# Optimization experiments

Measured on AMD Instinct MI355X. Metric: run time of the kernel, lower is better.

The kernel has to match this reference:

```python
import jax, jax.numpy as jnp
import numpy as np

C1 = 384  # input channel dim (hardcoded in source)


def setup_inputs() -> dict:
    key = jax.random.key(0)
    kx, kq, kk, kv = jax.random.split(key, 4)
    B, T, C, H = 512, 256, C1, 64
    x = jax.random.normal(kx, (B, T, C), dtype=jnp.float32)
    # nn.Linear(C1, head_size, bias=False) weights, stored as (C, H) for x @ W
    Wq = jax.random.normal(kq, (C, H), dtype=jnp.float32) * (1.0 / np.sqrt(C))
    Wk = jax.random.normal(kk, (C, H), dtype=jnp.float32) * (1.0 / np.sqrt(C))
    Wv = jax.random.normal(kv, (C, H), dtype=jnp.float32) * (1.0 / np.sqrt(C))
    return {"x": x, "Wq": Wq, "Wk": Wk, "Wv": Wv}


def reference(x, Wq, Wk, Wv):
    B, T, C = x.shape
    q = jnp.einsum('btc,ch->bth', x, Wq)  # [B,T,H]
    k = jnp.einsum('btc,ch->bth', x, Wk)
    v = jnp.einsum('btc,ch->bth', x, Wv)
    # NOTE: source MULTIPLIES by C**0.5 (not the usual 1/sqrt(d)) -- faithful.
    scale = jnp.asarray(C, x.dtype) ** 0.5
    wei = jnp.einsum('bth,bsh->bts', q, k) * scale  # [B,T,T]
    causal = jnp.tril(jnp.ones((T, T), dtype=bool))
    wei = jnp.where(causal, wei, -jnp.inf)
    wei = jax.nn.softmax(wei, axis=-1)
    # dropout is identity in eval mode (deterministic reference)
    out = jnp.einsum('bts,bsh->bth', wei, v)  # [B,T,H]
    return out
```

## Files before the change

### kernel.cpp

```cpp
#include <hip/hip_runtime.h>
#include <hip/hip_bf16.h>
#include <math.h>

typedef _Float16 f16x8 __attribute__((ext_vector_type(8)));
typedef _Float16 f16x4 __attribute__((ext_vector_type(4)));
typedef _Float16 f16x2 __attribute__((ext_vector_type(2)));
typedef __fp16 fp16x2 __attribute__((ext_vector_type(2)));
typedef float f32x4 __attribute__((ext_vector_type(4)));

#define MFMA16(a, b, c) __builtin_amdgcn_mfma_f32_16x16x32_f16((a), (b), (c), 0, 0, 0)

typedef __attribute__((address_space(3))) char as3_char;
typedef __attribute__((address_space(1))) const char as1_char;
__device__ __forceinline__ void glds16(const void* g, void* l) {
  __builtin_amdgcn_global_load_lds((as1_char*)g, (as3_char*)l, 16, 0, 0);
}

union F16x8u { f16x8 v; f16x2 h[4]; };

__device__ __forceinline__ f16x2 pkrtz(float a, float b) {
  fp16x2 r = __builtin_amdgcn_cvt_pkrtz(a, b);
  return __builtin_bit_cast(f16x2, r);
}

__global__ __launch_bounds__(256) void wprep_kernel(
    const float* __restrict__ Wq, const float* __restrict__ Wk, const float* __restrict__ Wv,
    _Float16* __restrict__ wstg) {
  int s = blockIdx.x * 256 + threadIdx.x;
  int c0 = s / 1536, s2 = s % 1536;
  int p = s2 / 768, r = (s2 % 768) / 4, gg = s2 & 3;
  int g = gg ^ ((r >> 1) & 3);
  int sel = r >> 6, h = r & 63;
  const float* W = (sel == 0) ? Wq : (sel == 1) ? Wk : Wv;
  f16x8 o;
#pragma unroll
  for (int e = 0; e < 8; ++e) {
    float val = W[(c0 * 32 + g * 8 + e) * 64 + h];
    _Float16 hi = (_Float16)val;
    o[e] = p ? (_Float16)(val - (float)hi) : hi;
  }
  *(f16x8*)&wstg[(size_t)s * 8] = o;
}

__global__ __launch_bounds__(1024) void fused_kernel(
    const float* __restrict__ x,
    const _Float16* __restrict__ wstg,
    float* __restrict__ out) {
  __shared__ __align__(16) char smem[156672];
  _Float16* kh = (_Float16*)smem;
  _Float16* kl = (_Float16*)(smem + 36864);
  _Float16* vT = (_Float16*)(smem + 73728);
  char* wbuf0 = smem + 107520;
  char* wbuf1 = smem + 132096;
  _Float16* slc = (_Float16*)(smem + 107520);

  const int tid = threadIdx.x;
  const int wave = tid >> 6, lane = tid & 63;
  const int g = lane >> 4, l16 = lane & 15;
  const int b = blockIdx.x;
  const int rs = 16 * wave;
  const int qr = rs + l16;
  const float* xb = x + (size_t)b * 98304;

  const float K2 = 28.270933f;
  const float NINF = -__builtin_inff();

  const float* xrow = xb + (size_t)qr * 384 + g * 8;

  f32x4 qa[4] = {}, ka[4] = {}, va[4] = {};
  float4 buf[3][2];

  if (wave < 12) {
#pragma unroll
    for (int i = 0; i < 2; ++i) {
      int seg0 = wave * 128 + i * 64;
      glds16(wstg + (size_t)(seg0 + lane) * 8, wbuf0 + seg0 * 16);
    }
  }
  __builtin_amdgcn_sched_barrier(0);
#pragma unroll
  for (int p = 0; p < 2; ++p) {
    buf[p][0] = *(const float4*)(xrow + p * 32);
    buf[p][1] = *(const float4*)(xrow + p * 32 + 4);
  }
  __builtin_amdgcn_sched_barrier(0);
  asm volatile("s_waitcnt vmcnt(2) lgkmcnt(0)" ::: "memory");
  __builtin_amdgcn_s_barrier();
  __builtin_amdgcn_sched_barrier(0);

#pragma unroll
  for (int c = 0; c < 12; ++c) {
    if (wave < 12 && c < 11) {
      char* nb = ((c + 1) & 1) ? wbuf1 : wbuf0;
      const _Float16* src = wstg + (size_t)(c + 1) * 12288;
#pragma unroll
      for (int i = 0; i < 2; ++i) {
        int seg0 = wave * 128 + i * 64;
        glds16(src + (size_t)(seg0 + lane) * 8, nb + seg0 * 16);
      }
    }
    __builtin_amdgcn_sched_barrier(0);
    if (c < 10) {
      buf[(c + 2) % 3][0] = *(const float4*)(xrow + (c + 2) * 32);
      buf[(c + 2) % 3][1] = *(const float4*)(xrow + (c + 2) * 32 + 4);
    }
    __builtin_amdgcn_sched_barrier(0);

    const char* wb = (c & 1) ? wbuf1 : wbuf0;
    f16x8 ah, al;
    {
      float vv[8] = {buf[c % 3][0].x, buf[c % 3][0].y, buf[c % 3][0].z,
                     buf[c % 3][0].w, buf[c % 3][1].x, buf[c % 3][1].y,
                     buf[c % 3][1].z, buf[c % 3][1].w};
      F16x8u uh, ul;
#pragma unroll
      for (int k2 = 0; k2 < 4; ++k2) {
        float a = vv[2 * k2], bb = vv[2 * k2 + 1];
        f16x2 hp = pkrtz(a, bb);
        uh.h[k2] = hp;
        ul.h[k2] = pkrtz(a - (float)hp[0], bb - (float)hp[1]);
      }
      ah = uh.v;
      al = ul.v;
    }
#pragma unroll
    for (int ct = 0; ct < 4; ++ct) {
      const int rq = ct * 16 + l16;
      const int rk = 64 + ct * 16 + l16;
      const int rv = 128 + ct * 16 + l16;
      f16x8 bqh = *(const f16x8*)(wb + (0 * 768 + rq * 4 + (g ^ ((rq >> 1) & 3))) * 16);
      f16x8 bql = *(const f16x8*)(wb + (1 * 768 + rq * 4 + (g ^ ((rq >> 1) & 3))) * 16);
      f16x8 bkh = *(const f16x8*)(wb + (0 * 768 + rk * 4 + (g ^ ((rk >> 1) & 3))) * 16);
      f16x8 bkl = *(const f16x8*)(wb + (1 * 768 + rk * 4 + (g ^ ((rk >> 1) & 3))) * 16);
      f16x8 bvh = *(const f16x8*)(wb + (0 * 768 + rv * 4 + (g ^ ((rv >> 1) & 3))) * 16);
      __builtin_amdgcn_s_setprio(1);
      qa[ct] = MFMA16(ah, bqh, qa[ct]);
      qa[ct] = MFMA16(al, bqh, qa[ct]);
      qa[ct] = MFMA16(ah, bql, qa[ct]);
      ka[ct] = MFMA16(ah, bkh, ka[ct]);
      ka[ct] = MFMA16(al, bkh, ka[ct]);
      ka[ct] = MFMA16(ah, bkl, ka[ct]);
      va[ct] = MFMA16(ah, bvh, va[ct]);
      __builtin_amdgcn_s_setprio(0);
    }
    if (c < 10) {
      asm volatile("s_waitcnt vmcnt(2) lgkmcnt(0)" ::: "memory");
    } else if (c == 10) {
      asm volatile("s_waitcnt vmcnt(0) lgkmcnt(0)" ::: "memory");
    } else {
      asm volatile("s_waitcnt lgkmcnt(0)" ::: "memory");
    }
    __builtin_amdgcn_s_barrier();
    __builtin_amdgcn_sched_barrier(0);
  }

#pragma unroll
  for (int ct = 0; ct < 4; ++ct) {
    const int h = ct * 16 + l16;
#pragma unroll
    for (int j = 0; j < 4; ++j) {
      const int row = rs + 4 * g + j;
      float kv = ka[ct][j];
      _Float16 khv = (_Float16)kv;
      kh[row * 72 + h] = khv;
      kl[row * 72 + h] = (_Float16)(kv - (float)khv);
      vT[h * 264 + row] = (_Float16)va[ct][j];
    }
  }
  __syncthreads();

  _Float16* myq = slc + (wave & 7) * 2304;
  f16x8 qhf[2], qlf[2];
#pragma unroll
  for (int rnd = 0; rnd < 2; ++rnd) {
    if ((wave >> 3) == rnd) {
#pragma unroll
      for (int ct = 0; ct < 4; ++ct) {
        const int h = ct * 16 + l16;
#pragma unroll
        for (int j = 0; j < 4; ++j) {
          const int rl = 4 * g + j;
          float qv = qa[ct][j];
          _Float16 qh = (_Float16)qv;
          myq[(rl * 2 + 0) * 72 + h] = qh;
          myq[(rl * 2 + 1) * 72 + h] = (_Float16)(qv - (float)qh);
        }
      }
    }
    __syncthreads();
    if ((wave >> 3) == rnd) {
#pragma unroll
      for (int ks = 0; ks < 2; ++ks) {
        qhf[ks] = *(const f16x8*)&myq[(l16 * 2 + 0) * 72 + ks * 32 + g * 8];
        qlf[ks] = *(const f16x8*)&myq[(l16 * 2 + 1) * 72 + ks * 32 + g * 8];
      }
    }
    __syncthreads();
  }
  asm volatile("s_waitcnt lgkmcnt(0)" ::: "memory");
  __builtin_amdgcn_sched_barrier(0);

  _Float16* psl = slc + wave * 1152;
  float mrun = NINF, srun = 0.f;
  f32x4 O[4] = {};

  for (int c = 0; c < 4; ++c) {
    const int kb = c * 64;
    if (kb > rs + 15) continue;
    f32x4 sa[4] = {};
#pragma unroll
    for (int kt = 0; kt < 4; ++kt) {
      const int kr = kb + 16 * kt;
      if (kr > rs + 15) continue;
#pragma unroll
      for (int ks = 0; ks < 2; ++ks) {
        const int ko = (kr + l16) * 72 + ks * 32 + g * 8;
        f16x8 akh = *(const f16x8*)&kh[ko];
        f16x8 akl = *(const f16x8*)&kl[ko];
        __builtin_amdgcn_s_setprio(1);
        sa[kt] = MFMA16(akh, qhf[ks], sa[kt]);
        sa[kt] = MFMA16(akl, qhf[ks], sa[kt]);
        sa[kt] = MFMA16(akh, qlf[ks], sa[kt]);
        __builtin_amdgcn_s_setprio(0);
      }
    }
    float cm = NINF;
#pragma unroll
    for (int kt = 0; kt < 4; ++kt)
#pragma unroll
      for (int j = 0; j < 4; ++j) {
        const int krow = kb + 16 * kt + 4 * g + j;
        float sv = (krow <= qr) ? sa[kt][j] : NINF;
        sa[kt][j] = sv;
        cm = fmaxf(cm, sv);
      }
    cm = fmaxf(cm, __shfl_xor(cm, 16));
    cm = fmaxf(cm, __shfl_xor(cm, 32));
    const float mn = fmaxf(mrun, cm);
    const float scl = exp2f(K2 * (mrun - mn));
    mrun = mn;
    float cs = 0.f;
#pragma unroll
    for (int kt = 0; kt < 4; ++kt)
#pragma unroll
      for (int j = 0; j < 4; ++j) {
        float p = exp2f(K2 * (sa[kt][j] - mn));
        cs += p;
        psl[l16 * 72 + kt * 16 + 4 * g + j] = (_Float16)p;
      }
    cs += __shfl_xor(cs, 16);
    cs += __shfl_xor(cs, 32);
    srun = srun * scl + cs;
#pragma unroll
    for (int ht = 0; ht < 4; ++ht) O[ht] *= scl;
    asm volatile("s_waitcnt lgkmcnt(0)" ::: "memory");
    __builtin_amdgcn_sched_barrier(0);
#pragma unroll
    for (int ks2 = 0; ks2 < 2; ++ks2) {
      f16x8 bp = *(const f16x8*)&psl[l16 * 72 + ks2 * 32 + g * 8];
#pragma unroll
      for (int ht = 0; ht < 4; ++ht) {
        f16x8 av = *(const f16x8*)&vT[(ht * 16 + l16) * 264 + kb + ks2 * 32 + g * 8];
        __builtin_amdgcn_s_setprio(1);
        O[ht] = MFMA16(av, bp, O[ht]);
        __builtin_amdgcn_s_setprio(0);
      }
    }
  }

  const float inv = 1.0f / srun;
#pragma unroll
  for (int ht = 0; ht < 4; ++ht) {
    f32x4 r = O[ht] * inv;
    *(f32x4*)&out[((size_t)b * 256 + qr) * 64 + ht * 16 + 4 * g] = r;
  }
}

extern "C" void kernel_launch(void* const* d_in, const int* in_sizes, int n_in,
                              void* d_out, int out_size, void* d_ws, size_t ws_size,
                              hipStream_t stream) {
  const float* x  = (const float*)d_in[0];
  const float* Wq = (const float*)d_in[1];
  const float* Wk = (const float*)d_in[2];
  const float* Wv = (const float*)d_in[3];

  _Float16* wstg = (_Float16*)d_ws;

  wprep_kernel<<<72, 256, 0, stream>>>(Wq, Wk, Wv, wstg);
  fused_kernel<<<512, 1024, 0, stream>>>(x, wstg, (float*)d_out);
}
```

Measured before the change: 81.63 us.

## Retile QKV projection as 2x2 row/column wave grid to halve weight LDS reads

The projection phase now gives each wave a 32-row by 32-column tile (two 16-row slabs times two 16-column tiles) instead of a 16-row by full-64-column tile. Each weight fragment read from LDS is reused across two row slabs, so per-wave LDS weight traffic is halved. The cost is that x is now loaded twice across column-group waves, the x prefetch is only double-buffered with a full vmcnt(0) wait each step, and the Q/K/V scatter to shared memory is remapped to the new row/column ownership.

```diff
diff --git a/kernel.cpp b/kernel.cpp
--- a/kernel.cpp
+++ b/kernel.cpp
@@ -58,17 +58,17 @@
   const int wave = tid >> 6, lane = tid & 63;
   const int g = lane >> 4, l16 = lane & 15;
   const int b = blockIdx.x;
-  const int rs = 16 * wave;
-  const int qr = rs + l16;
+  const int rg = wave & 7, cg = wave >> 3;
   const float* xb = x + (size_t)b * 98304;
 
   const float K2 = 28.270933f;
   const float NINF = -__builtin_inff();
 
-  const float* xrow = xb + (size_t)qr * 384 + g * 8;
-
-  f32x4 qa[4] = {}, ka[4] = {}, va[4] = {};
-  float4 buf[3][2];
+  const float* xrowA = xb + (size_t)(32 * rg + l16) * 384 + g * 8;
+  const float* xrowB = xrowA + 16 * 384;
+
+  f32x4 qa[2][2] = {}, ka[2][2] = {}, va[2][2] = {};
+  float4 buf[2][2][2];
 
   if (wave < 12) {
 #pragma unroll
@@ -78,13 +78,12 @@
     }
   }
   __builtin_amdgcn_sched_barrier(0);
-#pragma unroll
-  for (int p = 0; p < 2; ++p) {
-    buf[p][0] = *(const float4*)(xrow + p * 32);
-    buf[p][1] = *(const float4*)(xrow + p * 32 + 4);
-  }
-  __builtin_amdgcn_sched_barrier(0);
-  asm volatile("s_waitcnt vmcnt(2) lgkmcnt(0)" ::: "memory");
+  buf[0][0][0] = *(const float4*)(xrowA);
+  buf[0][0][1] = *(const float4*)(xrowA + 4);
+  buf[0][1][0] = *(const float4*)(xrowB);
+  buf[0][1][1] = *(const float4*)(xrowB + 4);
+  __builtin_amdgcn_sched_barrier(0);
+  asm volatile("s_waitcnt vmcnt(0) lgkmcnt(0)" ::: "memory");
   __builtin_amdgcn_s_barrier();
   __builtin_amdgcn_sched_barrier(0);
 
@@ -100,18 +99,21 @@
       }
     }
     __builtin_amdgcn_sched_barrier(0);
-    if (c < 10) {
-      buf[(c + 2) % 3][0] = *(const float4*)(xrow + (c + 2) * 32);
-      buf[(c + 2) % 3][1] = *(const float4*)(xrow + (c + 2) * 32 + 4);
+    if (c < 11) {
+      buf[(c + 1) & 1][0][0] = *(const float4*)(xrowA + (c + 1) * 32);
+      buf[(c + 1) & 1][0][1] = *(const float4*)(xrowA + (c + 1) * 32 + 4);
+      buf[(c + 1) & 1][1][0] = *(const float4*)(xrowB + (c + 1) * 32);
+      buf[(c + 1) & 1][1][1] = *(const float4*)(xrowB + (c + 1) * 32 + 4);
     }
     __builtin_amdgcn_sched_barrier(0);
 
     const char* wb = (c & 1) ? wbuf1 : wbuf0;
-    f16x8 ah, al;
-    {
-      float vv[8] = {buf[c % 3][0].x, buf[c % 3][0].y, buf[c % 3][0].z,
-                     buf[c % 3][0].w, buf[c % 3][1].x, buf[c % 3][1].y,
-                     buf[c % 3][1].z, buf[c % 3][1].w};
+    f16x8 ah[2], al[2];
+#pragma unroll
+    for (int s = 0; s < 2; ++s) {
+      float vv[8] = {buf[c & 1][s][0].x, buf[c & 1][s][0].y, buf[c & 1][s][0].z,
+                     buf[c & 1][s][0].w, buf[c & 1][s][1].x, buf[c & 1][s][1].y,
+                     buf[c & 1][s][1].z, buf[c & 1][s][1].w};
       F16x8u uh, ul;
 #pragma unroll
       for (int k2 = 0; k2 < 4; ++k2) {
@@ -120,79 +122,84 @@
         uh.h[k2] = hp;
         ul.h[k2] = pkrtz(a - (float)hp[0], bb - (float)hp[1]);
       }
-      ah = uh.v;
-      al = ul.v;
-    }
-#pragma unroll
-    for (int ct = 0; ct < 4; ++ct) {
-      const int rq = ct * 16 + l16;
-      const int rk = 64 + ct * 16 + l16;
-      const int rv = 128 + ct * 16 + l16;
+      ah[s] = uh.v;
+      al[s] = ul.v;
+    }
+#pragma unroll
+    for (int ct = 0; ct < 2; ++ct) {
+      const int rq = cg * 32 + ct * 16 + l16;
+      const int rk = 64 + rq;
+      const int rv = 128 + rq;
       f16x8 bqh = *(const f16x8*)(wb + (0 * 768 + rq * 4 + (g ^ ((rq >> 1) & 3))) * 16);
       f16x8 bql = *(const f16x8*)(wb + (1 * 768 + rq * 4 + (g ^ ((rq >> 1) & 3))) * 16);
       f16x8 bkh = *(const f16x8*)(wb + (0 * 768 + rk * 4 + (g ^ ((rk >> 1) & 3))) * 16);
       f16x8 bkl = *(const f16x8*)(wb + (1 * 768 + rk * 4 + (g ^ ((rk >> 1) & 3))) * 16);
       f16x8 bvh = *(const f16x8*)(wb + (0 * 768 + rv * 4 + (g ^ ((rv >> 1) & 3))) * 16);
       __builtin_amdgcn_s_setprio(1);
-      qa[ct] = MFMA16(ah, bqh, qa[ct]);
-      qa[ct] = MFMA16(al, bqh, qa[ct]);
-      qa[ct] = MFMA16(ah, bql, qa[ct]);
-      ka[ct] = MFMA16(ah, bkh, ka[ct]);
-      ka[ct] = MFMA16(al, bkh, ka[ct]);
-      ka[ct] = MFMA16(ah, bkl, ka[ct]);
-      va[ct] = MFMA16(ah, bvh, va[ct]);
+#pragma unroll
+      for (int s = 0; s < 2; ++s) {
+        qa[s][ct] = MFMA16(ah[s], bqh, qa[s][ct]);
+        qa[s][ct] = MFMA16(al[s], bqh, qa[s][ct]);
+        qa[s][ct] = MFMA16(ah[s], bql, qa[s][ct]);
+        ka[s][ct] = MFMA16(ah[s], bkh, ka[s][ct]);
+        ka[s][ct] = MFMA16(al[s], bkh, ka[s][ct]);
+        ka[s][ct] = MFMA16(ah[s], bkl, ka[s][ct]);
+        va[s][ct] = MFMA16(ah[s], bvh, va[s][ct]);
+      }
       __builtin_amdgcn_s_setprio(0);
     }
-    if (c < 10) {
-      asm volatile("s_waitcnt vmcnt(2) lgkmcnt(0)" ::: "memory");
-    } else if (c == 10) {
-      asm volatile("s_waitcnt vmcnt(0) lgkmcnt(0)" ::: "memory");
-    } else {
-      asm volatile("s_waitcnt lgkmcnt(0)" ::: "memory");
-    }
+    asm volatile("s_waitcnt vmcnt(0) lgkmcnt(0)" ::: "memory");
     __builtin_amdgcn_s_barrier();
     __builtin_amdgcn_sched_barrier(0);
   }
 
 #pragma unroll
-  for (int ct = 0; ct < 4; ++ct) {
-    const int h = ct * 16 + l16;
-#pragma unroll
-    for (int j = 0; j < 4; ++j) {
-      const int row = rs + 4 * g + j;
-      float kv = ka[ct][j];
-      _Float16 khv = (_Float16)kv;
-      kh[row * 72 + h] = khv;
-      kl[row * 72 + h] = (_Float16)(kv - (float)khv);
-      vT[h * 264 + row] = (_Float16)va[ct][j];
+  for (int s = 0; s < 2; ++s) {
+#pragma unroll
+    for (int ct = 0; ct < 2; ++ct) {
+      const int h = cg * 32 + ct * 16 + l16;
+#pragma unroll
+      for (int j = 0; j < 4; ++j) {
+        const int row = 32 * rg + 16 * s + 4 * g + j;
+        float kv = ka[s][ct][j];
+        _Float16 khv = (_Float16)kv;
+        kh[row * 72 + h] = khv;
+        kl[row * 72 + h] = (_Float16)(kv - (float)khv);
+        vT[h * 264 + row] = (_Float16)va[s][ct][j];
+      }
     }
   }
   __syncthreads();
 
-  _Float16* myq = slc + (wave & 7) * 2304;
+  _Float16* qsl = slc;
+  const int rs = 16 * wave;
+  const int qr = rs + l16;
   f16x8 qhf[2], qlf[2];
 #pragma unroll
   for (int rnd = 0; rnd < 2; ++rnd) {
-    if ((wave >> 3) == rnd) {
-#pragma unroll
-      for (int ct = 0; ct < 4; ++ct) {
-        const int h = ct * 16 + l16;
-#pragma unroll
-        for (int j = 0; j < 4; ++j) {
-          const int rl = 4 * g + j;
-          float qv = qa[ct][j];
-          _Float16 qh = (_Float16)qv;
-          myq[(rl * 2 + 0) * 72 + h] = qh;
-          myq[(rl * 2 + 1) * 72 + h] = (_Float16)(qv - (float)qh);
+    if ((rg >> 2) == rnd) {
+#pragma unroll
+      for (int s = 0; s < 2; ++s)
+#pragma unroll
+        for (int ct = 0; ct < 2; ++ct) {
+          const int f = cg * 32 + ct * 16 + l16;
+#pragma unroll
+          for (int j = 0; j < 4; ++j) {
+            const int rowp = (32 * rg + 16 * s + 4 * g + j) & 127;
+            float qv = qa[s][ct][j];
+            _Float16 qh16 = (_Float16)qv;
+            qsl[(rowp * 2 + 0) * 72 + f] = qh16;
+            qsl[(rowp * 2 + 1) * 72 + f] = (_Float16)(qv - (float)qh16);
+          }
         }
-      }
     }
     __syncthreads();
     if ((wave >> 3) == rnd) {
 #pragma unroll
       for (int ks = 0; ks < 2; ++ks) {
-        qhf[ks] = *(const f16x8*)&myq[(l16 * 2 + 0) * 72 + ks * 32 + g * 8];
-        qlf[ks] = *(const f16x8*)&myq[(l16 * 2 + 1) * 72 + ks * 32 + g * 8];
+        const int ro = ((rs & 127) + l16) * 2;
+        qhf[ks] = *(const f16x8*)&qsl[(ro + 0) * 72 + ks * 32 + g * 8];
+        qlf[ks] = *(const f16x8*)&qsl[(ro + 1) * 72 + ks * 32 + g * 8];
       }
     }
     __syncthreads();
```

After: 118.0 us. +44.6%, slower.

## Double K-chunk size in QKV projection loop and vectorize P stores

Applied to the files above, without the earlier changes.

The QKV projection loop now walks 6 chunks of 64 input channels instead of 12 chunks of 32. All 16 waves share the weight staging, and the two weight buffers are moved to the start of shared memory, overlapping the later K/V region. This halves the number of barriers and waitcnt points in the projection phase. The softmax probability write now packs four values with cvt_pkrtz into one f16x4 store instead of four scalar stores. In exchange, the x register buffer drops from three stages to two and waits fully on vmcnt(0) every iteration, which may expose more global-load latency.

```diff
diff --git a/kernel.cpp b/kernel.cpp
--- a/kernel.cpp
+++ b/kernel.cpp
@@ -46,12 +46,12 @@
     const float* __restrict__ x,
     const _Float16* __restrict__ wstg,
     float* __restrict__ out) {
-  __shared__ __align__(16) char smem[156672];
+  __shared__ __align__(16) char smem[147456];
+  char* wbuf0 = smem;
+  char* wbuf1 = smem + 49152;
   _Float16* kh = (_Float16*)smem;
   _Float16* kl = (_Float16*)(smem + 36864);
   _Float16* vT = (_Float16*)(smem + 73728);
-  char* wbuf0 = smem + 107520;
-  char* wbuf1 = smem + 132096;
   _Float16* slc = (_Float16*)(smem + 107520);
 
   const int tid = threadIdx.x;
@@ -68,84 +68,87 @@
   const float* xrow = xb + (size_t)qr * 384 + g * 8;
 
   f32x4 qa[4] = {}, ka[4] = {}, va[4] = {};
-  float4 buf[3][2];
-
-  if (wave < 12) {
-#pragma unroll
-    for (int i = 0; i < 2; ++i) {
-      int seg0 = wave * 128 + i * 64;
-      glds16(wstg + (size_t)(seg0 + lane) * 8, wbuf0 + seg0 * 16);
-    }
-  }
-  __builtin_amdgcn_sched_barrier(0);
-#pragma unroll
-  for (int p = 0; p < 2; ++p) {
-    buf[p][0] = *(const float4*)(xrow + p * 32);
-    buf[p][1] = *(const float4*)(xrow + p * 32 + 4);
-  }
-  __builtin_amdgcn_sched_barrier(0);
-  asm volatile("s_waitcnt vmcnt(2) lgkmcnt(0)" ::: "memory");
+  float4 buf[2][2][2];
+
+#pragma unroll
+  for (int i = 0; i < 3; ++i) {
+    int seg0 = wave * 192 + i * 64;
+    glds16(wstg + (size_t)(seg0 + lane) * 8, wbuf0 + seg0 * 16);
+  }
+  __builtin_amdgcn_sched_barrier(0);
+#pragma unroll
+  for (int ks = 0; ks < 2; ++ks) {
+    buf[0][ks][0] = *(const float4*)(xrow + ks * 32);
+    buf[0][ks][1] = *(const float4*)(xrow + ks * 32 + 4);
+  }
+  __builtin_amdgcn_sched_barrier(0);
+  asm volatile("s_waitcnt vmcnt(0) lgkmcnt(0)" ::: "memory");
   __builtin_amdgcn_s_barrier();
   __builtin_amdgcn_sched_barrier(0);
 
 #pragma unroll
-  for (int c = 0; c < 12; ++c) {
-    if (wave < 12 && c < 11) {
+  for (int c = 0; c < 6; ++c) {
+    if (c < 5) {
       char* nb = ((c + 1) & 1) ? wbuf1 : wbuf0;
-      const _Float16* src = wstg + (size_t)(c + 1) * 12288;
-#pragma unroll
-      for (int i = 0; i < 2; ++i) {
-        int seg0 = wave * 128 + i * 64;
+      const _Float16* src = wstg + (size_t)(c + 1) * 24576;
+#pragma unroll
+      for (int i = 0; i < 3; ++i) {
+        int seg0 = wave * 192 + i * 64;
         glds16(src + (size_t)(seg0 + lane) * 8, nb + seg0 * 16);
       }
     }
     __builtin_amdgcn_sched_barrier(0);
-    if (c < 10) {
-      buf[(c + 2) % 3][0] = *(const float4*)(xrow + (c + 2) * 32);
-      buf[(c + 2) % 3][1] = *(const float4*)(xrow + (c + 2) * 32 + 4);
+    if (c < 5) {
+#pragma unroll
+      for (int ks = 0; ks < 2; ++ks) {
+        buf[(c + 1) & 1][ks][0] = *(const float4*)(xrow + (c + 1) * 64 + ks * 32);
+        buf[(c + 1) & 1][ks][1] = *(const float4*)(xrow + (c + 1) * 64 + ks * 32 + 4);
+      }
     }
     __builtin_amdgcn_sched_barrier(0);
 
     const char* wb = (c & 1) ? wbuf1 : wbuf0;
-    f16x8 ah, al;
-    {
-      float vv[8] = {buf[c % 3][0].x, buf[c % 3][0].y, buf[c % 3][0].z,
-                     buf[c % 3][0].w, buf[c % 3][1].x, buf[c % 3][1].y,
-                     buf[c % 3][1].z, buf[c % 3][1].w};
-      F16x8u uh, ul;
-#pragma unroll
-      for (int k2 = 0; k2 < 4; ++k2) {
-        float a = vv[2 * k2], bb = vv[2 * k2 + 1];
-        f16x2 hp = pkrtz(a, bb);
-        uh.h[k2] = hp;
-        ul.h[k2] = pkrtz(a - (float)hp[0], bb - (float)hp[1]);
-      }
-      ah = uh.v;
-      al = ul.v;
-    }
-#pragma unroll
-    for (int ct = 0; ct < 4; ++ct) {
-      const int rq = ct * 16 + l16;
-      const int rk = 64 + ct * 16 + l16;
-      const int rv = 128 + ct * 16 + l16;
-      f16x8 bqh = *(const f16x8*)(wb + (0 * 768 + rq * 4 + (g ^ ((rq >> 1) & 3))) * 16);
-      f16x8 bql = *(const f16x8*)(wb + (1 * 768 + rq * 4 + (g ^ ((rq >> 1) & 3))) * 16);
-      f16x8 bkh = *(const f16x8*)(wb + (0 * 768 + rk * 4 + (g ^ ((rk >> 1) & 3))) * 16);
-      f16x8 bkl = *(const f16x8*)(wb + (1 * 768 + rk * 4 + (g ^ ((rk >> 1) & 3))) * 16);
-      f16x8 bvh = *(const f16x8*)(wb + (0 * 768 + rv * 4 + (g ^ ((rv >> 1) & 3))) * 16);
-      __builtin_amdgcn_s_setprio(1);
-      qa[ct] = MFMA16(ah, bqh, qa[ct]);
-      qa[ct] = MFMA16(al, bqh, qa[ct]);
-      qa[ct] = MFMA16(ah, bql, qa[ct]);
-      ka[ct] = MFMA16(ah, bkh, ka[ct]);
-      ka[ct] = MFMA16(al, bkh, ka[ct]);
-      ka[ct] = MFMA16(ah, bkl, ka[ct]);
-      va[ct] = MFMA16(ah, bvh, va[ct]);
-      __builtin_amdgcn_s_setprio(0);
-    }
-    if (c < 10) {
-      asm volatile("s_waitcnt vmcnt(2) lgkmcnt(0)" ::: "memory");
-    } else if (c == 10) {
+#pragma unroll
+    for (int ks = 0; ks < 2; ++ks) {
+      const char* wbk = wb + ks * 24576;
+      f16x8 ah, al;
+      {
+        float vv[8] = {buf[c & 1][ks][0].x, buf[c & 1][ks][0].y, buf[c & 1][ks][0].z,
+                       buf[c & 1][ks][0].w, buf[c & 1][ks][1].x, buf[c & 1][ks][1].y,
+                       buf[c & 1][ks][1].z, buf[c & 1][ks][1].w};
+        F16x8u uh, ul;
+#pragma unroll
+        for (int k2 = 0; k2 < 4; ++k2) {
+          float a = vv[2 * k2], bb = vv[2 * k2 + 1];
+          f16x2 hp = pkrtz(a, bb);
+          uh.h[k2] = hp;
+          ul.h[k2] = pkrtz(a - (float)hp[0], bb - (float)hp[1]);
+        }
+        ah = uh.v;
+        al = ul.v;
+      }
+#pragma unroll
+      for (int ct = 0; ct < 4; ++ct) {
+        const int rq = ct * 16 + l16;
+        const int rk = 64 + rq;
+        const int rv = 128 + rq;
+        f16x8 bqh = *(const f16x8*)(wbk + (0 * 768 + rq * 4 + (g ^ ((rq >> 1) & 3))) * 16);
+        f16x8 bql = *(const f16x8*)(wbk + (1 * 768 + rq * 4 + (g ^ ((rq >> 1) & 3))) * 16);
+        f16x8 bkh = *(const f16x8*)(wbk + (0 * 768 + rk * 4 + (g ^ ((rk >> 1) & 3))) * 16);
+        f16x8 bkl = *(const f16x8*)(wbk + (1 * 768 + rk * 4 + (g ^ ((rk >> 1) & 3))) * 16);
+        f16x8 bvh = *(const f16x8*)(wbk + (0 * 768 + rv * 4 + (g ^ ((rv >> 1) & 3))) * 16);
+        __builtin_amdgcn_s_setprio(1);
+        qa[ct] = MFMA16(ah, bqh, qa[ct]);
+        qa[ct] = MFMA16(al, bqh, qa[ct]);
+        qa[ct] = MFMA16(ah, bql, qa[ct]);
+        ka[ct] = MFMA16(ah, bkh, ka[ct]);
+        ka[ct] = MFMA16(al, bkh, ka[ct]);
+        ka[ct] = MFMA16(ah, bkl, ka[ct]);
+        va[ct] = MFMA16(ah, bvh, va[ct]);
+        __builtin_amdgcn_s_setprio(0);
+      }
+    }
+    if (c < 5) {
       asm volatile("s_waitcnt vmcnt(0) lgkmcnt(0)" ::: "memory");
     } else {
       asm volatile("s_waitcnt lgkmcnt(0)" ::: "memory");
@@ -241,13 +244,16 @@
     mrun = mn;
     float cs = 0.f;
 #pragma unroll
-    for (int kt = 0; kt < 4; ++kt)
-#pragma unroll
-      for (int j = 0; j < 4; ++j) {
-        float p = exp2f(K2 * (sa[kt][j] - mn));
-        cs += p;
-        psl[l16 * 72 + kt * 16 + 4 * g + j] = (_Float16)p;
-      }
+    for (int kt = 0; kt < 4; ++kt) {
+      float p0 = exp2f(K2 * (sa[kt][0] - mn));
+      float p1 = exp2f(K2 * (sa[kt][1] - mn));
+      float p2 = exp2f(K2 * (sa[kt][2] - mn));
+      float p3 = exp2f(K2 * (sa[kt][3] - mn));
+      cs += (p0 + p1) + (p2 + p3);
+      f16x2 lo2 = pkrtz(p0, p1), hi2 = pkrtz(p2, p3);
+      f16x4 pk = {lo2[0], lo2[1], hi2[0], hi2[1]};
+      *(f16x4*)&psl[l16 * 72 + kt * 16 + 4 * g] = pk;
+    }
     cs += __shfl_xor(cs, 16);
     cs += __shfl_xor(cs, 32);
     srun = srun * scl + cs;
```

After: 88.84 us. 8.8% more time.
